# Kernel optimization log

Measured on AMD Instinct MI355X. Metric: run time of the kernel, lower is better.

## Reference

```python
import jax, jax.numpy as jnp
import numpy as np

N, E, D_IN, H, OUT = 50000, 800000, 128, 256, 2
BN_EPS = 1e-5
LN_EPS = 1e-5


def _xavier(k, fi, fo):
    lim = float(np.sqrt(6.0 / (fi + fo)))
    return jax.random.uniform(k, (fi, fo), minval=-lim, maxval=lim, dtype=jnp.float32)


def setup_inputs() -> dict:
    key = jax.random.key(0)
    ks = jax.random.split(key, 8)
    return {
        "x": jax.random.normal(ks[0], (N, D_IN), dtype=jnp.float32),
        "edge_index": jax.random.randint(ks[1], (2, E), 0, N, dtype=jnp.int32),
        "feature_scale": jnp.ones((D_IN,), jnp.float32),
        "feature_bias": jnp.zeros((D_IN,), jnp.float32),
        "bn0_g": jnp.ones((D_IN,), jnp.float32),
        "bn0_b": jnp.zeros((D_IN,), jnp.float32),
        "W1": _xavier(ks[2], D_IN, H), "b1": jnp.zeros((H,), jnp.float32),
        "bn1_g": jnp.ones((H,), jnp.float32), "bn1_b": jnp.zeros((H,), jnp.float32),
        "ln1_g": jnp.ones((H,), jnp.float32), "ln1_b": jnp.zeros((H,), jnp.float32),
        "W2": _xavier(ks[3], H, H), "b2": jnp.zeros((H,), jnp.float32),
        "bn2_g": jnp.ones((H,), jnp.float32), "bn2_b": jnp.zeros((H,), jnp.float32),
        "ln2_g": jnp.ones((H,), jnp.float32), "ln2_b": jnp.zeros((H,), jnp.float32),
        "Wout": _xavier(ks[4], H, OUT), "bout": jnp.zeros((OUT,), jnp.float32),
    }


def _batchnorm(x, g, b):
    # training-mode BatchNorm1d: batch stats over node axis, biased variance
    mu = jnp.mean(x, axis=0)
    var = jnp.mean(jnp.square(x - mu), axis=0)
    return g * (x - mu) * jax.lax.rsqrt(var + BN_EPS) + b


def _layernorm(x, g, b):
    mu = jnp.mean(x, axis=-1, keepdims=True)
    var = jnp.mean(jnp.square(x - mu), axis=-1, keepdims=True)
    return g * (x - mu) * jax.lax.rsqrt(var + LN_EPS) + b


def _gcn(x, W, b, src, dst, dinv):
    # PyG GCNConv with self-loops: D^{-1/2}(A+I)D^{-1/2} X W + b
    h = x @ W                                   # [N, F]
    norm = (dinv[src] * dinv[dst])[:, None]     # [E, 1]
    msg = h[src] * norm                         # [E, F] (dominant traffic)
    agg = jax.ops.segment_sum(msg, dst, num_segments=N)
    return agg + (dinv * dinv)[:, None] * h + b


def _forward(x, feature_scale, feature_bias, bn0_g, bn0_b,
             W1, b1, bn1_g, bn1_b, ln1_g, ln1_b,
             W2, b2, bn2_g, bn2_b, ln2_g, ln2_b,
             Wout, bout, edge_index):
    src, dst = edge_index[0], edge_index[1]
    deg = jax.ops.segment_sum(jnp.ones((E,), x.dtype), dst, num_segments=N) + 1.0
    dinv = jax.lax.rsqrt(deg)

    h = x * feature_scale + feature_bias
    h = _batchnorm(h, bn0_g, bn0_b)            # input_bn; dropout = identity (eval)

    # layer 0 (no residual: i == 0)
    h1 = _gcn(h, W1, b1, src, dst, dinv)
    h1 = jax.nn.relu(h1)
    h1 = _batchnorm(h1, bn1_g, bn1_b)
    h1 = _layernorm(h1, ln1_g, ln1_b)

    # layer 1 (residual add, shapes match)
    h2 = _gcn(h1, W2, b2, src, dst, dinv)
    h2 = jax.nn.relu(h2)
    h2 = _batchnorm(h2, bn2_g, bn2_b)
    h2 = _layernorm(h2, ln2_g, ln2_b)
    h2 = h2 + h1

    return h2 @ Wout + bout


def reference(x, edge_index, feature_scale, feature_bias, bn0_g, bn0_b,
              W1, b1, bn1_g, bn1_b, ln1_g, ln1_b,
              W2, b2, bn2_g, bn2_b, ln2_g, ln2_b,
              Wout, bout):
    return _forward(x, feature_scale, feature_bias, bn0_g, bn0_b,
                    W1, b1, bn1_g, bn1_b, ln1_g, ln1_b,
                    W2, b2, bn2_g, bn2_b, ln2_g, ln2_b,
                    Wout, bout, edge_index)
```

## Files before the change

### kernel.cpp

```cpp
#include <hip/hip_runtime.h>
#include <hip/hip_bf16.h>
#include <stdint.h>

#define N_NODES 50000
#define N_EDGES 800000
#define D_IN    128
#define H_DIM   256
#define BN_EPS  1e-5f
#define LN_EPS  1e-5f
#define NBLK2 782
#define SLICE_ELEMS ((size_t)N_NODES * 32)
#define EDGE_CHUNK 4096
#define BN0_BLOCKS 1024
#define TR_BLOCKS 256
#define NBKT 196
#define CHUNK 2048
#define RCHUNKS 391

typedef float v4f __attribute__((ext_vector_type(4)));
typedef float v2f __attribute__((ext_vector_type(2)));
typedef short v8s __attribute__((ext_vector_type(8)));
typedef unsigned v4u __attribute__((ext_vector_type(4)));

__device__ __forceinline__ float bflo(unsigned u){ return __uint_as_float(u << 16); }
__device__ __forceinline__ float bfhi(unsigned u){ return __uint_as_float(u & 0xffff0000u); }
__device__ __forceinline__ unsigned short f2bf(float f){
  unsigned u = __float_as_uint(f);
  u += 0x7fffu + ((u >> 16) & 1u);
  return (unsigned short)(u >> 16);
}
__device__ __forceinline__ unsigned pack2(float a, float b){
  return (unsigned)f2bf(a) | ((unsigned)f2bf(b) << 16);
}

__device__ __forceinline__ int block_excl_scan(int v){
  int t = threadIdx.x;
  int lane = t & 63, w = t >> 6;
  int inc = v;
  #pragma unroll
  for (int m = 1; m < 64; m <<= 1){
    int o = __shfl_up(inc, m, 64);
    if (lane >= m) inc += o;
  }
  __shared__ int wsum[4];
  if (lane == 63) wsum[w] = inc;
  __syncthreads();
  int base = 0;
  #pragma unroll
  for (int j = 0; j < 4; ++j) if (j < w) base += wsum[j];
  return base + inc - v;
}

__global__ __launch_bounds__(256) void bn0r1_k(const int* ei, const float* x,
                                               const float* fs, const float* fb,
                                               float* S, float* Q, int* ghist){
  int b = blockIdx.x, t = threadIdx.x;
  if (b >= BN0_BLOCKS){
    __shared__ int lh[NBKT];
    int b2 = b - BN0_BLOCKS;
    for (int i = t; i < NBKT; i += 256) lh[i] = 0;
    __syncthreads();
    int e0 = b2 * CHUNK;
    int n = min(CHUNK, N_EDGES - e0);
    for (int i = t; i < n; i += 256)
      atomicAdd(&lh[ei[N_EDGES + e0 + i] >> 8], 1);
    __syncthreads();
    if (t < NBKT && lh[t] > 0) atomicAdd(&ghist[t], lh[t]);
    return;
  }
  int cl = t & 31, rg = t >> 5;
  int c = cl * 4;
  float4 fs4 = *(const float4*)(fs + c);
  float4 fb4 = *(const float4*)(fb + c);
  float s0=0,s1=0,s2=0,s3=0,q0=0,q1=0,q2=0,q3=0;
  for (int row = b * 8 + rg; row < N_NODES; row += BN0_BLOCKS * 8){
    float4 xv = *(const float4*)(x + (size_t)row * D_IN + c);
    float v0 = xv.x * fs4.x + fb4.x;
    float v1 = xv.y * fs4.y + fb4.y;
    float v2 = xv.z * fs4.z + fb4.z;
    float v3 = xv.w * fs4.w + fb4.w;
    s0 += v0; s1 += v1; s2 += v2; s3 += v3;
    q0 += v0*v0; q1 += v1*v1; q2 += v2*v2; q3 += v3*v3;
  }
  __shared__ float red[256][8];
  red[t][0]=s0; red[t][1]=s1; red[t][2]=s2; red[t][3]=s3;
  red[t][4]=q0; red[t][5]=q1; red[t][6]=q2; red[t][7]=q3;
  __syncthreads();
  float* Sr = S + (b & 7) * D_IN;
  float* Qr = Q + (b & 7) * D_IN;
  if (t < 32){
    float a[8];
    #pragma unroll
    for (int i = 0; i < 8; ++i) a[i] = red[t][i];
    for (int j = 1; j < 8; ++j)
      #pragma unroll
      for (int i = 0; i < 8; ++i) a[i] += red[t + 32*j][i];
    #pragma unroll
    for (int i = 0; i < 4; ++i){ atomicAdd(&Sr[t*4+i], a[i]); atomicAdd(&Qr[t*4+i], a[4+i]); }
  }
}

__global__ __launch_bounds__(256) void r3_k(const int* ei, const int* ghist, int* gcursor, unsigned* ebuf){
  __shared__ unsigned short dstS[CHUNK];
  __shared__ int lh[NBKT], cb[NBKT], sbb[NBKT];
  int t = threadIdx.x;
  int v = (t < NBKT) ? ghist[t] : 0;
  int epre = block_excl_scan(v);
  if (t < NBKT){ sbb[t] = epre; lh[t] = 0; }
  __syncthreads();
  int e0 = blockIdx.x * CHUNK;
  int n = min(CHUNK, N_EDGES - e0);
  for (int i = t; i < n; i += 256){
    int d = ei[N_EDGES + e0 + i];
    dstS[i] = (unsigned short)d;
    atomicAdd(&lh[d >> 8], 1);
  }
  __syncthreads();
  if (t < NBKT && lh[t] > 0) cb[t] = sbb[t] + atomicAdd(&gcursor[t], lh[t]);
  __syncthreads();
  if (t < NBKT) lh[t] = 0;
  __syncthreads();
  for (int i = t; i < n; i += 256){
    int d = dstS[i];
    int bkt = d >> 8;
    int r = atomicAdd(&lh[bkt], 1);
    unsigned src = (unsigned)ei[e0 + i];
    ebuf[cb[bkt] + r] = ((unsigned)(d & 255) << 16) | src;
  }
}

__global__ __launch_bounds__(256) void sortprep_k(const unsigned* ebuf, const int* ghist,
                                                  int* perm, int* offs, float* dinv,
                                                  unsigned short* edges,
                                                  const float* W1, const float* W2,
                                                  unsigned short* W1t, unsigned short* W2t){
  int b = blockIdx.x, t = threadIdx.x;
  if (b < NBKT){
    __shared__ int h[256], dh[128], ep_s[128], W_s[128], lc[128], curs[256], sbb[NBKT + 1];
    int gv = (t < NBKT) ? ghist[t] : 0;
    int gpre = block_excl_scan(gv);
    if (t < NBKT) sbb[t] = gpre;
    if (t == NBKT - 1) sbb[NBKT] = gpre + gv;
    h[t] = 0;
    if (t < 128){ dh[t] = 0; lc[t] = 0; }
    __syncthreads();
    int lo = sbb[b], hi = sbb[b + 1];
    for (int i = lo + t; i < hi; i += 256)
      atomicAdd(&h[(ebuf[i] >> 16) & 255], 1);
    __syncthreads();
    int node = b * 256 + t;
    bool valid = node < N_NODES;
    int deg = valid ? h[t] : 0;
    if (valid) atomicAdd(&dh[min(deg, 127)], 1);
    __syncthreads();
    int cv = (t < 128) ? dh[t] : 0;
    int e1 = block_excl_scan(cv);
    __syncthreads();
    int e2 = block_excl_scan((t < 128) ? cv * t : 0);
    __syncthreads();
    if (t < 128){ ep_s[t] = e1; W_s[t] = e2; }
    __syncthreads();
    if (valid){
      int bin = min(deg, 127);
      int r = atomicAdd(&lc[bin], 1);
      int pl = ep_s[bin] + r;
      int pos = b * 256 + pl;
      int off = lo + W_s[bin] + (pl - ep_s[bin]) * deg;
      perm[pos] = node;
      offs[pos] = off;
      dinv[node] = rsqrtf((float)deg + 1.0f);
      curs[t] = off;
    }
    __syncthreads();
    for (int i = lo + t; i < hi; i += 256){
      unsigned u = ebuf[i];
      int l8 = (u >> 16) & 255;
      int pos = atomicAdd(&curs[l8], 1);
      edges[pos] = (unsigned short)(u & 0xffffu);
    }
    if (b == 0 && t == 0) offs[N_NODES] = N_EDGES;
    return;
  }
  int i = (b - NBKT) * 256 + t;
  if (i < D_IN * H_DIM){
    int r = i / H_DIM, c = i % H_DIM;
    W1t[c * D_IN + r] = f2bf(W1[i]);
  }
  if (i < H_DIM * H_DIM){
    int r = i / H_DIM, c = i % H_DIM;
    W2t[c * H_DIM + r] = f2bf(W2[i]);
  }
}

__global__ __launch_bounds__(256) void gemm1_k(const float* x, const float* S, const float* Q,
                                               const float* fs, const float* fb,
                                               const float* gg, const float* bb,
                                               const unsigned short* Bt, const float* dinv,
                                               unsigned short* C, int M){
  __shared__ __align__(16) short smem[18944];
  __shared__ float ac[128], cc[128], dvs[64];
  short* As = smem;
  short* Bs = smem + 64 * 136;
  int t = threadIdx.x;
  int m0 = blockIdx.x * 64;
  int lane = t & 63, w = t >> 6;
  int fr = lane & 15, quad = lane >> 4;
  if (t < 64) dvs[t] = (m0 + t < M) ? dinv[m0 + t] : 0.0f;
  if (t < 128){
    float s8 = 0.f, q8 = 0.f;
    #pragma unroll
    for (int rep = 0; rep < 8; ++rep){ s8 += S[rep * D_IN + t]; q8 += Q[rep * D_IN + t]; }
    const float invN = 1.0f / N_NODES;
    float mu = s8 * invN;
    float rs = rsqrtf(q8 * invN - mu * mu + BN_EPS);
    float a = gg[t] * rs * fs[t];
    ac[t] = a;
    cc[t] = gg[t] * rs * (fb[t] - mu) + bb[t];
  }
  __syncthreads();
  {
    int r = t >> 2, q = t & 3;
    int arow = m0 + r;
    #pragma unroll
    for (int j = 0; j < 4; ++j){
      int c = q * 32 + j * 8;
      float4 xv0 = {0,0,0,0}, xv1 = {0,0,0,0};
      if (arow < M){
        xv0 = *(const float4*)(x + (size_t)arow * D_IN + c);
        xv1 = *(const float4*)(x + (size_t)arow * D_IN + c + 4);
      }
      float4 a0 = *(const float4*)(&ac[c]);
      float4 a1 = *(const float4*)(&ac[c + 4]);
      float4 c0 = *(const float4*)(&cc[c]);
      float4 c1 = *(const float4*)(&cc[c + 4]);
      uint4 o;
      o.x = pack2(a0.x * xv0.x + c0.x, a0.y * xv0.y + c0.y);
      o.y = pack2(a0.z * xv0.z + c0.z, a0.w * xv0.w + c0.w);
      o.z = pack2(a1.x * xv1.x + c1.x, a1.y * xv1.y + c1.y);
      o.w = pack2(a1.z * xv1.z + c1.z, a1.w * xv1.w + c1.w);
      *(uint4*)(&As[r * 136 + c]) = o;
    }
  }
  v4f acc[4][4] = {};
  int sr = t >> 2;
  int sk = (t & 3) << 3;
  for (int k0 = 0; k0 < D_IN; k0 += 32){
    __syncthreads();
    #pragma unroll
    for (int j = 0; j < 4; ++j){
      int brow = sr + 64 * j;
      uint4 bv = *(const uint4*)(Bt + (size_t)brow * D_IN + k0 + sk);
      *(uint4*)(&Bs[brow * 40 + sk]) = bv;
    }
    __syncthreads();
    v8s af[4], bf[4];
    #pragma unroll
    for (int mi = 0; mi < 4; ++mi)
      af[mi] = *(const v8s*)(&As[(mi * 16 + fr) * 136 + k0 + quad * 8]);
    #pragma unroll
    for (int ni = 0; ni < 4; ++ni)
      bf[ni] = *(const v8s*)(&Bs[(w * 64 + ni * 16 + fr) * 40 + quad * 8]);
    #pragma unroll
    for (int mi = 0; mi < 4; ++mi)
      #pragma unroll
      for (int ni = 0; ni < 4; ++ni)
        acc[mi][ni] = __builtin_amdgcn_mfma_f32_16x16x32_bf16(af[mi], bf[ni], acc[mi][ni], 0, 0, 0);
  }
  __syncthreads();
  short* Cs = smem;
  #pragma unroll
  for (int mi = 0; mi < 4; ++mi)
    #pragma unroll
    for (int ni = 0; ni < 4; ++ni)
      #pragma unroll
      for (int r = 0; r < 4; ++r){
        int row = mi * 16 + quad * 4 + r;
        int col = w * 64 + ni * 16 + fr;
        Cs[row * 264 + col] = (short)f2bf(acc[mi][ni][r] * dvs[row]);
      }
  __syncthreads();
  int orow = t >> 2;
  int grow = m0 + orow;
  if (grow < M){
    #pragma unroll
    for (int j = 0; j < 4; ++j){
      int oc = (t & 3) * 16 + 64 * j;
      v8s v0 = *(const v8s*)(&Cs[orow * 264 + oc]);
      v8s v1 = *(const v8s*)(&Cs[orow * 264 + oc + 8]);
      *(v8s*)(&C[(size_t)(oc >> 5) * SLICE_ELEMS + (size_t)grow * 32 + (oc & 31)]) = v0;
      int oc1 = oc + 8;
      *(v8s*)(&C[(size_t)(oc1 >> 5) * SLICE_ELEMS + (size_t)grow * 32 + (oc1 & 31)]) = v1;
    }
  }
}

__global__ __launch_bounds__(256) void gemm2_k(const unsigned short* gB,
                                               const float* Sg, const float* Qg,
                                               const float* bng, const float* bnb,
                                               const float* lng, const float* lnb,
                                               const unsigned short* Bt, const float* dinv,
                                               unsigned short* C, unsigned short* h1, int M){
  __shared__ __align__(16) short smem[27136];
  __shared__ float scs[256], shs[256], dvs[64];
  short* As = smem;
  short* Bs = smem + 64 * 264;
  int t = threadIdx.x;
  int m0 = blockIdx.x * 64;
  int lane = t & 63, w = t >> 6;
  int fr = lane & 15, quad = lane >> 4;
  if (t < 64) dvs[t] = (m0 + t < M) ? dinv[m0 + t] : 0.0f;
  {
    const float invN = 1.0f / N_NODES;
    float mu = Sg[t] * invN;
    float rs = rsqrtf(Qg[t] * invN - mu * mu + BN_EPS);
    float s = bng[t] * rs;
    scs[t] = s; shs[t] = bnb[t] - s * mu;
  }
  __syncthreads();
  {
    int r = t >> 2, q = t & 3;
    int grow = m0 + r;
    int c0 = q * 64;
    float v[64];
    #pragma unroll
    for (int j = 0; j < 8; ++j){
      uint4 u = {0,0,0,0};
      int c = c0 + j * 8;
      if (grow < M) u = *(const uint4*)(gB + (size_t)grow * H_DIM + c);
      float4 s0 = *(const float4*)(&scs[c]);
      float4 s1 = *(const float4*)(&scs[c + 4]);
      float4 h0 = *(const float4*)(&shs[c]);
      float4 h4 = *(const float4*)(&shs[c + 4]);
      v[j*8+0] = s0.x * bflo(u.x) + h0.x;
      v[j*8+1] = s0.y * bfhi(u.x) + h0.y;
      v[j*8+2] = s0.z * bflo(u.y) + h0.z;
      v[j*8+3] = s0.w * bfhi(u.y) + h0.w;
      v[j*8+4] = s1.x * bflo(u.z) + h4.x;
      v[j*8+5] = s1.y * bfhi(u.z) + h4.y;
      v[j*8+6] = s1.z * bflo(u.w) + h4.z;
      v[j*8+7] = s1.w * bfhi(u.w) + h4.w;
    }
    float sum = 0.f, sq = 0.f;
    #pragma unroll
    for (int i = 0; i < 64; ++i){ sum += v[i]; sq += v[i] * v[i]; }
    sum += __shfl_xor(sum, 1, 64); sum += __shfl_xor(sum, 2, 64);
    sq  += __shfl_xor(sq, 1, 64);  sq  += __shfl_xor(sq, 2, 64);
    float mu = sum * (1.0f / H_DIM);
    float var = sq * (1.0f / H_DIM) - mu * mu;
    float rs = rsqrtf(var + LN_EPS);
    #pragma unroll
    for (int j = 0; j < 8; ++j){
      int c = c0 + j * 8;
      float4 g0 = *(const float4*)(lng + c);
      float4 g1 = *(const float4*)(lng + c + 4);
      float4 b0 = *(const float4*)(lnb + c);
      float4 b1 = *(const float4*)(lnb + c + 4);
      uint4 o;
      o.x = pack2(g0.x * (v[j*8+0] - mu) * rs + b0.x, g0.y * (v[j*8+1] - mu) * rs + b0.y);
      o.y = pack2(g0.z * (v[j*8+2] - mu) * rs + b0.z, g0.w * (v[j*8+3] - mu) * rs + b0.w);
      o.z = pack2(g1.x * (v[j*8+4] - mu) * rs + b1.x, g1.y * (v[j*8+5] - mu) * rs + b1.y);
      o.w = pack2(g1.z * (v[j*8+6] - mu) * rs + b1.z, g1.w * (v[j*8+7] - mu) * rs + b1.w);
      *(uint4*)(&As[r * 264 + c]) = o;
      if (grow < M) *(uint4*)(h1 + (size_t)grow * H_DIM + c) = o;
    }
  }
  v4f acc[4][4] = {};
  int sr = t >> 2;
  int sk = (t & 3) << 3;
  for (int k0 = 0; k0 < H_DIM; k0 += 32){
    __syncthreads();
    #pragma unroll
    for (int j = 0; j < 4; ++j){
      int brow = sr + 64 * j;
      uint4 bv = *(const uint4*)(Bt + (size_t)brow * H_DIM + k0 + sk);
      *(uint4*)(&Bs[brow * 40 + sk]) = bv;
    }
    __syncthreads();
    v8s af[4], bf[4];
    #pragma unroll
    for (int mi = 0; mi < 4; ++mi)
      af[mi] = *(const v8s*)(&As[(mi * 16 + fr) * 264 + k0 + quad * 8]);
    #pragma unroll
    for (int ni = 0; ni < 4; ++ni)
      bf[ni] = *(const v8s*)(&Bs[(w * 64 + ni * 16 + fr) * 40 + quad * 8]);
    #pragma unroll
    for (int mi = 0; mi < 4; ++mi)
      #pragma unroll
      for (int ni = 0; ni < 4; ++ni)
        acc[mi][ni] = __builtin_amdgcn_mfma_f32_16x16x32_bf16(af[mi], bf[ni], acc[mi][ni], 0, 0, 0);
  }
  __syncthreads();
  short* Cs = smem;
  #pragma unroll
  for (int mi = 0; mi < 4; ++mi)
    #pragma unroll
    for (int ni = 0; ni < 4; ++ni)
      #pragma unroll
      for (int r = 0; r < 4; ++r){
        int row = mi * 16 + quad * 4 + r;
        int col = w * 64 + ni * 16 + fr;
        Cs[row * 264 + col] = (short)f2bf(acc[mi][ni][r] * dvs[row]);
      }
  __syncthreads();
  int orow = t >> 2;
  int grow = m0 + orow;
  if (grow < M){
    #pragma unroll
    for (int j = 0; j < 4; ++j){
      int oc = (t & 3) * 16 + 64 * j;
      v8s v0 = *(const v8s*)(&Cs[orow * 264 + oc]);
      v8s v1 = *(const v8s*)(&Cs[orow * 264 + oc + 8]);
      *(v8s*)(&C[(size_t)(oc >> 5) * SLICE_ELEMS + (size_t)grow * 32 + (oc & 31)]) = v0;
      int oc1 = oc + 8;
      *(v8s*)(&C[(size_t)(oc1 >> 5) * SLICE_ELEMS + (size_t)grow * 32 + (oc1 & 31)]) = v1;
    }
  }
}

#define ACCP(u, A) { v2f d_ = {bflo(u), bfhi(u)}; A += d_; }
#define ACC8(vv) ACCP(vv.x, A0) ACCP(vv.y, A1) ACCP(vv.z, A2) ACCP(vv.w, A3)

__global__ __launch_bounds__(256, 4) void agg_k(const unsigned short* hs, const int* offsets,
                                                const unsigned short* edges, const int* perm,
                                                const float* dinv, const float* bias,
                                                unsigned short* g, float* pS, float* pQ){
  __shared__ unsigned eds32[EDGE_CHUNK / 2];
  __shared__ float wps[4][4][16];
  int t = threadIdx.x;
  int lane = t & 63;
  int wv = t >> 6;
  int slice = blockIdx.x & 7;
  int l4 = lane & 3;
  int grp = blockIdx.x >> 3;
  int nb = grp * 64;
  int idx = nb + (t >> 2);
  int lastn = min(nb + 64, N_NODES);
  int blk0 = offsets[nb];
  int base = blk0 & ~1;
  int blkN = offsets[lastn];
  const unsigned* gsrc = (const unsigned*)(edges + base);
  int nu = min((blkN - base + 1) >> 1, EDGE_CHUNK / 2);
  for (int i = t; i < nu; i += 256)
    eds32[i] = gsrc[i];
  __syncthreads();
  bool act = idx < N_NODES;
  int node = act ? perm[idx] : 0;
  float dvv = act ? dinv[node] : 0.f;
  const uint4* hb4 = (const uint4*)(hs + (size_t)slice * SLICE_ELEMS);
  float4 bb0 = *(const float4*)(bias + slice * 32 + l4 * 8);
  float4 bb1 = *(const float4*)(bias + slice * 32 + l4 * 8 + 4);
  uint4 sv = hb4[(size_t)node * 4 + l4];
  v2f A0 = {bflo(sv.x), bfhi(sv.x)};
  v2f A1 = {bflo(sv.y), bfhi(sv.y)};
  v2f A2 = {bflo(sv.z), bfhi(sv.z)};
  v2f A3 = {bflo(sv.w), bfhi(sv.w)};
  int e  = act ? offsets[idx] : 0;
  int e1 = act ? offsets[idx + 1] : 0;
  if ((e & 1) && e < e1){
    int ru = (e - base) >> 1;
    unsigned d = (ru < EDGE_CHUNK / 2) ? eds32[ru] : gsrc[ru];
    uint4 vv = hb4[(size_t)(d >> 16) * 4 + l4];
    ACC8(vv);
    ++e;
  }
  for (; e + 16 <= e1; e += 16){
    int ru = (e - base) >> 1;
    unsigned dd[8];
    if (ru + 8 <= EDGE_CHUNK / 2){
      #pragma unroll
      for (int j = 0; j < 8; ++j) dd[j] = eds32[ru + j];
    } else {
      #pragma unroll
      for (int j = 0; j < 8; ++j) dd[j] = gsrc[ru + j];
    }
    uint4 v[16];
    #pragma unroll
    for (int j = 0; j < 8; ++j){
      v[2*j]   = hb4[(size_t)(dd[j] & 0xffffu) * 4 + l4];
      v[2*j+1] = hb4[(size_t)(dd[j] >> 16)     * 4 + l4];
    }
    #pragma unroll
    for (int j = 0; j < 16; ++j){ ACC8(v[j]); }
  }
  if (e + 8 <= e1){
    int ru = (e - base) >> 1;
    unsigned dd[4];
    if (ru + 4 <= EDGE_CHUNK / 2){
      #pragma unroll
      for (int j = 0; j < 4; ++j) dd[j] = eds32[ru + j];
    } else {
      #pragma unroll
      for (int j = 0; j < 4; ++j) dd[j] = gsrc[ru + j];
    }
    uint4 v[8];
    #pragma unroll
    for (int j = 0; j < 4; ++j){
      v[2*j]   = hb4[(size_t)(dd[j] & 0xffffu) * 4 + l4];
      v[2*j+1] = hb4[(size_t)(dd[j] >> 16)     * 4 + l4];
    }
    #pragma unroll
    for (int j = 0; j < 8; ++j){ ACC8(v[j]); }
    e += 8;
  }
  if (e + 4 <= e1){
    int ru = (e - base) >> 1;
    unsigned dd0, dd1;
    if (ru + 2 <= EDGE_CHUNK / 2){
      dd0 = eds32[ru]; dd1 = eds32[ru + 1];
    } else {
      dd0 = gsrc[ru]; dd1 = gsrc[ru + 1];
    }
    uint4 v[4];
    v[0] = hb4[(size_t)(dd0 & 0xffffu) * 4 + l4];
    v[1] = hb4[(size_t)(dd0 >> 16)     * 4 + l4];
    v[2] = hb4[(size_t)(dd1 & 0xffffu) * 4 + l4];
    v[3] = hb4[(size_t)(dd1 >> 16)     * 4 + l4];
    #pragma unroll
    for (int j = 0; j < 4; ++j){ ACC8(v[j]); }
    e += 4;
  }
  for (; e < e1; ++e){
    int r = e - base;
    unsigned d = ((r >> 1) < EDGE_CHUNK / 2) ? eds32[r >> 1] : gsrc[r >> 1];
    unsigned s = (r & 1) ? (d >> 16) : (d & 0xffffu);
    uint4 vv = hb4[(size_t)s * 4 + l4];
    ACC8(vv);
  }
  float y0 = act ? fmaxf(dvv * A0.x + bb0.x, 0.f) : 0.f;
  float y1 = act ? fmaxf(dvv * A0.y + bb0.y, 0.f) : 0.f;
  float y2 = act ? fmaxf(dvv * A1.x + bb0.z, 0.f) : 0.f;
  float y3 = act ? fmaxf(dvv * A1.y + bb0.w, 0.f) : 0.f;
  float y4 = act ? fmaxf(dvv * A2.x + bb1.x, 0.f) : 0.f;
  float y5 = act ? fmaxf(dvv * A2.y + bb1.y, 0.f) : 0.f;
  float y6 = act ? fmaxf(dvv * A3.x + bb1.z, 0.f) : 0.f;
  float y7 = act ? fmaxf(dvv * A3.y + bb1.w, 0.f) : 0.f;
  if (act){
    v4u o;
    o.x = pack2(y0, y1); o.y = pack2(y2, y3);
    o.z = pack2(y4, y5); o.w = pack2(y6, y7);
    __builtin_nontemporal_store(o, (v4u*)(g + (size_t)node * H_DIM + slice * 32 + l4 * 8));
  }
  float q0 = y0*y0, q1 = y1*y1, q2 = y2*y2, q3 = y3*y3;
  float q4 = y4*y4, q5 = y5*y5, q6 = y6*y6, q7 = y7*y7;
  #pragma unroll
  for (int m = 4; m < 64; m <<= 1){
    y0 += __shfl_xor(y0, m, 64); y1 += __shfl_xor(y1, m, 64);
    y2 += __shfl_xor(y2, m, 64); y3 += __shfl_xor(y3, m, 64);
    y4 += __shfl_xor(y4, m, 64); y5 += __shfl_xor(y5, m, 64);
    y6 += __shfl_xor(y6, m, 64); y7 += __shfl_xor(y7, m, 64);
    q0 += __shfl_xor(q0, m, 64); q1 += __shfl_xor(q1, m, 64);
    q2 += __shfl_xor(q2, m, 64); q3 += __shfl_xor(q3, m, 64);
    q4 += __shfl_xor(q4, m, 64); q5 += __shfl_xor(q5, m, 64);
    q6 += __shfl_xor(q6, m, 64); q7 += __shfl_xor(q7, m, 64);
  }
  if (lane < 4){
    wps[wv][lane][0] = y0; wps[wv][lane][1] = y1; wps[wv][lane][2] = y2; wps[wv][lane][3] = y3;
    wps[wv][lane][4] = y4; wps[wv][lane][5] = y5; wps[wv][lane][6] = y6; wps[wv][lane][7] = y7;
    wps[wv][lane][8] = q0; wps[wv][lane][9] = q1; wps[wv][lane][10] = q2; wps[wv][lane][11] = q3;
    wps[wv][lane][12] = q4; wps[wv][lane][13] = q5; wps[wv][lane][14] = q6; wps[wv][lane][15] = q7;
  }
  __syncthreads();
  if (t < 64){
    int tl = t >> 4, ti = t & 15;
    float v = wps[0][tl][ti] + wps[1][tl][ti] + wps[2][tl][ti] + wps[3][tl][ti];
    int col32 = tl * 8 + (ti & 7);
    if (ti < 8) pS[(size_t)blockIdx.x * 32 + col32] = v;
    else        pQ[(size_t)blockIdx.x * 32 + col32] = v;
  }
}

__global__ __launch_bounds__(1024) void redu_k(const float* pS, const float* pQ,
                                               float* Sg, float* Qg){
  __shared__ float ls[32][32], lq[32][32];
  int t = threadIdx.x;
  int slice = blockIdx.x & 7;
  int part = blockIdx.x >> 3;
  int grp = t >> 5, c32 = t & 31;
  float as = 0.f, aq = 0.f;
  for (int b2 = part + grp * 8; b2 < NBLK2; b2 += 256){
    size_t o = ((size_t)b2 * 8 + slice) * 32 + c32;
    as += pS[o]; aq += pQ[o];
  }
  ls[grp][c32] = as; lq[grp][c32] = aq;
  __syncthreads();
  if (t < 32){
    float S = 0.f, Q = 0.f;
    #pragma unroll
    for (int gI = 0; gI < 32; ++gI){ S += ls[gI][t]; Q += lq[gI][t]; }
    atomicAdd(&Sg[slice * 32 + t], S);
    atomicAdd(&Qg[slice * 32 + t], Q);
  }
}

__global__ __launch_bounds__(256) void apply2_k(const unsigned short* g,
                                                const float* Sg, const float* Qg,
                                                const float* bng, const float* bnb,
                                                const float* lng, const float* lnb,
                                                const unsigned short* h1, const float* Wout,
                                                const float* bout, float* out){
  int t = threadIdx.x;
  int lane32 = t & 31;
  int row = blockIdx.x * 8 + (t >> 5);
  if (row >= N_NODES) return;
  int c = lane32 * 8;
  const float invN = 1.0f / N_NODES;
  float4 S0 = *(const float4*)(Sg + c), S1 = *(const float4*)(Sg + c + 4);
  float4 Q0 = *(const float4*)(Qg + c), Q1 = *(const float4*)(Qg + c + 4);
  float4 G0 = *(const float4*)(bng + c), G1 = *(const float4*)(bng + c + 4);
  float4 B0 = *(const float4*)(bnb + c), B1 = *(const float4*)(bnb + c + 4);
  float Sa[8] = {S0.x,S0.y,S0.z,S0.w,S1.x,S1.y,S1.z,S1.w};
  float Qa[8] = {Q0.x,Q0.y,Q0.z,Q0.w,Q1.x,Q1.y,Q1.z,Q1.w};
  float Ga[8] = {G0.x,G0.y,G0.z,G0.w,G1.x,G1.y,G1.z,G1.w};
  float Ba[8] = {B0.x,B0.y,B0.z,B0.w,B1.x,B1.y,B1.z,B1.w};
  float scv[8], shv[8];
  #pragma unroll
  for (int j = 0; j < 8; ++j){
    float mu = Sa[j] * invN;
    float rs = rsqrtf(Qa[j] * invN - mu * mu + BN_EPS);
    float s = Ga[j] * rs;
    scv[j] = s; shv[j] = Ba[j] - s * mu;
  }
  uint4 u = *(const uint4*)(g + (size_t)row * H_DIM + c);
  float v0 = scv[0] * bflo(u.x) + shv[0];
  float v1 = scv[1] * bfhi(u.x) + shv[1];
  float v2 = scv[2] * bflo(u.y) + shv[2];
  float v3 = scv[3] * bfhi(u.y) + shv[3];
  float v4 = scv[4] * bflo(u.z) + shv[4];
  float v5 = scv[5] * bfhi(u.z) + shv[5];
  float v6 = scv[6] * bflo(u.w) + shv[6];
  float v7 = scv[7] * bfhi(u.w) + shv[7];
  float sum = v0+v1+v2+v3+v4+v5+v6+v7;
  float sq  = v0*v0+v1*v1+v2*v2+v3*v3+v4*v4+v5*v5+v6*v6+v7*v7;
  #pragma unroll
  for (int m = 1; m < 32; m <<= 1){ sum += __shfl_xor(sum, m, 64); sq += __shfl_xor(sq, m, 64); }
  float mu = sum * (1.0f / H_DIM);
  float var = sq * (1.0f / H_DIM) - mu * mu;
  float rs = rsqrtf(var + LN_EPS);
  float4 g40 = *(const float4*)(lng + c);
  float4 g41 = *(const float4*)(lng + c + 4);
  float4 b40 = *(const float4*)(lnb + c);
  float4 b41 = *(const float4*)(lnb + c + 4);
  uint4 hr = *(const uint4*)(h1 + (size_t)row * H_DIM + c);
  float y0 = g40.x * (v0 - mu) * rs + b40.x + bflo(hr.x);
  float y1 = g40.y * (v1 - mu) * rs + b40.y + bfhi(hr.x);
  float y2 = g40.z * (v2 - mu) * rs + b40.z + bflo(hr.y);
  float y3 = g40.w * (v3 - mu) * rs + b40.w + bfhi(hr.y);
  float y4 = g41.x * (v4 - mu) * rs + b41.x + bflo(hr.z);
  float y5 = g41.y * (v5 - mu) * rs + b41.y + bfhi(hr.z);
  float y6 = g41.z * (v6 - mu) * rs + b41.z + bflo(hr.w);
  float y7 = g41.w * (v7 - mu) * rs + b41.w + bfhi(hr.w);
  float4 w0 = *(const float4*)(Wout + c * 2);
  float4 w1 = *(const float4*)(Wout + c * 2 + 4);
  float4 w2 = *(const float4*)(Wout + c * 2 + 8);
  float4 w3 = *(const float4*)(Wout + c * 2 + 12);
  float o0 = y0*w0.x + y1*w0.z + y2*w1.x + y3*w1.z + y4*w2.x + y5*w2.z + y6*w3.x + y7*w3.z;
  float o1 = y0*w0.y + y1*w0.w + y2*w1.y + y3*w1.w + y4*w2.y + y5*w2.w + y6*w3.y + y7*w3.w;
  #pragma unroll
  for (int m = 1; m < 32; m <<= 1){ o0 += __shfl_xor(o0, m, 64); o1 += __shfl_xor(o1, m, 64); }
  if (lane32 == 0){
    out[(size_t)row * 2 + 0] = o0 + bout[0];
    out[(size_t)row * 2 + 1] = o1 + bout[1];
  }
}

extern "C" void kernel_launch(void* const* d_in, const int* in_sizes, int n_in,
                              void* d_out, int out_size, void* d_ws, size_t ws_size,
                              hipStream_t stream) {
  const float* x    = (const float*)d_in[0];
  const int*   ei   = (const int*)d_in[1];
  const float* fs   = (const float*)d_in[2];
  const float* fb   = (const float*)d_in[3];
  const float* bn0g = (const float*)d_in[4];
  const float* bn0b = (const float*)d_in[5];
  const float* W1   = (const float*)d_in[6];
  const float* b1   = (const float*)d_in[7];
  const float* bn1g = (const float*)d_in[8];
  const float* bn1b = (const float*)d_in[9];
  const float* ln1g = (const float*)d_in[10];
  const float* ln1b = (const float*)d_in[11];
  const float* W2   = (const float*)d_in[12];
  const float* b2   = (const float*)d_in[13];
  const float* bn2g = (const float*)d_in[14];
  const float* bn2b = (const float*)d_in[15];
  const float* ln2g = (const float*)d_in[16];
  const float* ln2b = (const float*)d_in[17];
  const float* Wout = (const float*)d_in[18];
  const float* bout = (const float*)d_in[19];
  float* out = (float*)d_out;

  char* w = (char*)d_ws;
  float* bn0S  = (float*)(w + 0);
  float* bn0Q  = (float*)(w + 4096);
  int*   ghist  = (int*)(w + 8192);
  int*   gcursor= (int*)(w + 8976);
  float* Sg1   = (float*)(w + 9760);
  float* Qg1   = (float*)(w + 10784);
  float* Sg2   = (float*)(w + 11808);
  float* Qg2   = (float*)(w + 12832);
  const size_t ZERO_BYTES = 13856;
  float* dinv  = (float*)(w + 211584);
  int*   offs  = (int*)(w + 411584);
  int*   perm  = (int*)(w + 611712);
  unsigned short* edges = (unsigned short*)(w + 1011712);
  unsigned short* W1t  = (unsigned short*)(w + 15411712);
  unsigned short* W2t  = (unsigned short*)(w + 15477248);
  unsigned short* hlin = (unsigned short*)(w + 15608320);
  unsigned*       ebuf = (unsigned*)(w + 15608320);
  unsigned short* gbuf = (unsigned short*)(w + 41208320);
  unsigned short* h1   = (unsigned short*)(w + 66808320);
  float* pS    = (float*)(w + 92408320);
  float* pQ    = (float*)(w + 94008832);

  (void)in_sizes; (void)n_in; (void)out_size; (void)ws_size;

  hipMemsetAsync(d_ws, 0, ZERO_BYTES, stream);

  bn0r1_k<<<BN0_BLOCKS + RCHUNKS, 256, 0, stream>>>(ei, x, fs, fb, bn0S, bn0Q, ghist);
  r3_k<<<RCHUNKS, 256, 0, stream>>>(ei, ghist, gcursor, ebuf);
  sortprep_k<<<NBKT + TR_BLOCKS, 256, 0, stream>>>(
      ebuf, ghist, perm, offs, dinv, edges, W1, W2, W1t, W2t);

  int ggrid = (N_NODES + 63) / 64;
  int agg_blocks = NBLK2 * 8;

  gemm1_k<<<ggrid, 256, 0, stream>>>(x, bn0S, bn0Q, fs, fb, bn0g, bn0b, W1t, dinv, hlin, N_NODES);
  agg_k<<<agg_blocks, 256, 0, stream>>>(hlin, offs, edges, perm, dinv, b1, gbuf, pS, pQ);
  redu_k<<<64, 1024, 0, stream>>>(pS, pQ, Sg1, Qg1);

  gemm2_k<<<ggrid, 256, 0, stream>>>(gbuf, Sg1, Qg1, bn1g, bn1b, ln1g, ln1b, W2t, dinv, hlin, h1, N_NODES);
  agg_k<<<agg_blocks, 256, 0, stream>>>(hlin, offs, edges, perm, dinv, b2, gbuf, pS, pQ);
  redu_k<<<64, 1024, 0, stream>>>(pS, pQ, Sg2, Qg2);
  apply2_k<<<(N_NODES + 7) / 8, 256, 0, stream>>>(gbuf, Sg2, Qg2, bn2g, bn2b, ln2g, ln2b, h1, Wout, bout, out);
}
```

Before: 360.3 us.

## Split BN1/LN1 prologue out of gemm2 into separate apply kernel

Removes the fused batchnorm+layernorm prologue from the second GEMM and moves it into a standalone elementwise kernel that writes h1. The GEMM becomes a generic templated kernel that streams A tiles from global memory with a smaller shared-memory footprint, which may allow higher occupancy. The trade-off is an extra launch plus a full write and re-read of h1 (N×256 bf16) through global memory.

```diff
diff --git a/kernel.cpp b/kernel.cpp
--- a/kernel.cpp
+++ b/kernel.cpp
@@ -294,92 +294,39 @@
   }
 }
 
-__global__ __launch_bounds__(256) void gemm2_k(const unsigned short* gB,
-                                               const float* Sg, const float* Qg,
-                                               const float* bng, const float* bnb,
-                                               const float* lng, const float* lnb,
-                                               const unsigned short* Bt, const float* dinv,
-                                               unsigned short* C, unsigned short* h1, int M){
-  __shared__ __align__(16) short smem[27136];
-  __shared__ float scs[256], shs[256], dvs[64];
+template<int K>
+__global__ __launch_bounds__(256) void gemm_k(const unsigned short* A, const unsigned short* Bt,
+                                              const float* dinv, unsigned short* C, int M){
+  __shared__ __align__(16) short smem[16896];
+  __shared__ float dvs[64];
   short* As = smem;
-  short* Bs = smem + 64 * 264;
+  short* Bs = smem + 64 * 40;
   int t = threadIdx.x;
   int m0 = blockIdx.x * 64;
-  int lane = t & 63, w = t >> 6;
+  int lane = t & 63;
+  int w = t >> 6;
   int fr = lane & 15, quad = lane >> 4;
   if (t < 64) dvs[t] = (m0 + t < M) ? dinv[m0 + t] : 0.0f;
-  {
-    const float invN = 1.0f / N_NODES;
-    float mu = Sg[t] * invN;
-    float rs = rsqrtf(Qg[t] * invN - mu * mu + BN_EPS);
-    float s = bng[t] * rs;
-    scs[t] = s; shs[t] = bnb[t] - s * mu;
-  }
-  __syncthreads();
-  {
-    int r = t >> 2, q = t & 3;
-    int grow = m0 + r;
-    int c0 = q * 64;
-    float v[64];
-    #pragma unroll
-    for (int j = 0; j < 8; ++j){
-      uint4 u = {0,0,0,0};
-      int c = c0 + j * 8;
-      if (grow < M) u = *(const uint4*)(gB + (size_t)grow * H_DIM + c);
-      float4 s0 = *(const float4*)(&scs[c]);
-      float4 s1 = *(const float4*)(&scs[c + 4]);
-      float4 h0 = *(const float4*)(&shs[c]);
-      float4 h4 = *(const float4*)(&shs[c + 4]);
-      v[j*8+0] = s0.x * bflo(u.x) + h0.x;
-      v[j*8+1] = s0.y * bfhi(u.x) + h0.y;
-      v[j*8+2] = s0.z * bflo(u.y) + h0.z;
-      v[j*8+3] = s0.w * bfhi(u.y) + h0.w;
-      v[j*8+4] = s1.x * bflo(u.z) + h4.x;
-      v[j*8+5] = s1.y * bfhi(u.z) + h4.y;
-      v[j*8+6] = s1.z * bflo(u.w) + h4.z;
-      v[j*8+7] = s1.w * bfhi(u.w) + h4.w;
-    }
-    float sum = 0.f, sq = 0.f;
-    #pragma unroll
-    for (int i = 0; i < 64; ++i){ sum += v[i]; sq += v[i] * v[i]; }
-    sum += __shfl_xor(sum, 1, 64); sum += __shfl_xor(sum, 2, 64);
-    sq  += __shfl_xor(sq, 1, 64);  sq  += __shfl_xor(sq, 2, 64);
-    float mu = sum * (1.0f / H_DIM);
-    float var = sq * (1.0f / H_DIM) - mu * mu;
-    float rs = rsqrtf(var + LN_EPS);
-    #pragma unroll
-    for (int j = 0; j < 8; ++j){
-      int c = c0 + j * 8;
-      float4 g0 = *(const float4*)(lng + c);
-      float4 g1 = *(const float4*)(lng + c + 4);
-      float4 b0 = *(const float4*)(lnb + c);
-      float4 b1 = *(const float4*)(lnb + c + 4);
-      uint4 o;
-      o.x = pack2(g0.x * (v[j*8+0] - mu) * rs + b0.x, g0.y * (v[j*8+1] - mu) * rs + b0.y);
-      o.y = pack2(g0.z * (v[j*8+2] - mu) * rs + b0.z, g0.w * (v[j*8+3] - mu) * rs + b0.w);
-      o.z = pack2(g1.x * (v[j*8+4] - mu) * rs + b1.x, g1.y * (v[j*8+5] - mu) * rs + b1.y);
-      o.w = pack2(g1.z * (v[j*8+6] - mu) * rs + b1.z, g1.w * (v[j*8+7] - mu) * rs + b1.w);
-      *(uint4*)(&As[r * 264 + c]) = o;
-      if (grow < M) *(uint4*)(h1 + (size_t)grow * H_DIM + c) = o;
-    }
-  }
   v4f acc[4][4] = {};
   int sr = t >> 2;
   int sk = (t & 3) << 3;
-  for (int k0 = 0; k0 < H_DIM; k0 += 32){
-    __syncthreads();
+  for (int k0 = 0; k0 < K; k0 += 32){
+    __syncthreads();
+    uint4 av = {0,0,0,0};
+    int arow = m0 + sr;
+    if (arow < M) av = *(const uint4*)(A + (size_t)arow * K + k0 + sk);
+    *(uint4*)(&As[sr * 40 + sk]) = av;
     #pragma unroll
     for (int j = 0; j < 4; ++j){
       int brow = sr + 64 * j;
-      uint4 bv = *(const uint4*)(Bt + (size_t)brow * H_DIM + k0 + sk);
+      uint4 bv = *(const uint4*)(Bt + (size_t)brow * K + k0 + sk);
       *(uint4*)(&Bs[brow * 40 + sk]) = bv;
     }
     __syncthreads();
     v8s af[4], bf[4];
     #pragma unroll
     for (int mi = 0; mi < 4; ++mi)
-      af[mi] = *(const v8s*)(&As[(mi * 16 + fr) * 264 + k0 + quad * 8]);
+      af[mi] = *(const v8s*)(&As[(mi * 16 + fr) * 40 + quad * 8]);
     #pragma unroll
     for (int ni = 0; ni < 4; ++ni)
       bf[ni] = *(const v8s*)(&Bs[(w * 64 + ni * 16 + fr) * 40 + quad * 8]);
@@ -590,6 +537,60 @@
     atomicAdd(&Sg[slice * 32 + t], S);
     atomicAdd(&Qg[slice * 32 + t], Q);
   }
+}
+
+__global__ __launch_bounds__(256) void apply1_k(const unsigned short* g,
+                                                const float* Sg, const float* Qg,
+                                                const float* bng, const float* bnb,
+                                                const float* lng, const float* lnb, unsigned short* h1){
+  int t = threadIdx.x;
+  int lane32 = t & 31;
+  int row = blockIdx.x * 8 + (t >> 5);
+  if (row >= N_NODES) return;
+  int c = lane32 * 8;
+  const float invN = 1.0f / N_NODES;
+  float4 S0 = *(const float4*)(Sg + c), S1 = *(const float4*)(Sg + c + 4);
+  float4 Q0 = *(const float4*)(Qg + c), Q1 = *(const float4*)(Qg + c + 4);
+  float4 G0 = *(const float4*)(bng + c), G1 = *(const float4*)(bng + c + 4);
+  float4 B0 = *(const float4*)(bnb + c), B1 = *(const float4*)(bnb + c + 4);
+  float Sa[8] = {S0.x,S0.y,S0.z,S0.w,S1.x,S1.y,S1.z,S1.w};
+  float Qa[8] = {Q0.x,Q0.y,Q0.z,Q0.w,Q1.x,Q1.y,Q1.z,Q1.w};
+  float Ga[8] = {G0.x,G0.y,G0.z,G0.w,G1.x,G1.y,G1.z,G1.w};
+  float Ba[8] = {B0.x,B0.y,B0.z,B0.w,B1.x,B1.y,B1.z,B1.w};
+  float scv[8], shv[8];
+  #pragma unroll
+  for (int j = 0; j < 8; ++j){
+    float mu = Sa[j] * invN;
+    float rs = rsqrtf(Qa[j] * invN - mu * mu + BN_EPS);
+    float s = Ga[j] * rs;
+    scv[j] = s; shv[j] = Ba[j] - s * mu;
+  }
+  uint4 u = *(const uint4*)(g + (size_t)row * H_DIM + c);
+  float v0 = scv[0] * bflo(u.x) + shv[0];
+  float v1 = scv[1] * bfhi(u.x) + shv[1];
+  float v2 = scv[2] * bflo(u.y) + shv[2];
+  float v3 = scv[3] * bfhi(u.y) + shv[3];
+  float v4 = scv[4] * bflo(u.z) + shv[4];
+  float v5 = scv[5] * bfhi(u.z) + shv[5];
+  float v6 = scv[6] * bflo(u.w) + shv[6];
+  float v7 = scv[7] * bfhi(u.w) + shv[7];
+  float sum = v0+v1+v2+v3+v4+v5+v6+v7;
+  float sq  = v0*v0+v1*v1+v2*v2+v3*v3+v4*v4+v5*v5+v6*v6+v7*v7;
+  #pragma unroll
+  for (int m = 1; m < 32; m <<= 1){ sum += __shfl_xor(sum, m, 64); sq += __shfl_xor(sq, m, 64); }
+  float mu = sum * (1.0f / H_DIM);
+  float var = sq * (1.0f / H_DIM) - mu * mu;
+  float rs = rsqrtf(var + LN_EPS);
+  float4 g40 = *(const float4*)(lng + c);
+  float4 g41 = *(const float4*)(lng + c + 4);
+  float4 b40 = *(const float4*)(lnb + c);
+  float4 b41 = *(const float4*)(lnb + c + 4);
+  uint4 o;
+  o.x = pack2(g40.x * (v0 - mu) * rs + b40.x, g40.y * (v1 - mu) * rs + b40.y);
+  o.y = pack2(g40.z * (v2 - mu) * rs + b40.z, g40.w * (v3 - mu) * rs + b40.w);
+  o.z = pack2(g41.x * (v4 - mu) * rs + b41.x, g41.y * (v5 - mu) * rs + b41.y);
+  o.w = pack2(g41.z * (v6 - mu) * rs + b41.z, g41.w * (v7 - mu) * rs + b41.w);
+  *(uint4*)(h1 + (size_t)row * H_DIM + c) = o;
 }
 
 __global__ __launch_bounds__(256) void apply2_k(const unsigned short* g,
@@ -726,8 +727,9 @@
   gemm1_k<<<ggrid, 256, 0, stream>>>(x, bn0S, bn0Q, fs, fb, bn0g, bn0b, W1t, dinv, hlin, N_NODES);
   agg_k<<<agg_blocks, 256, 0, stream>>>(hlin, offs, edges, perm, dinv, b1, gbuf, pS, pQ);
   redu_k<<<64, 1024, 0, stream>>>(pS, pQ, Sg1, Qg1);
-
-  gemm2_k<<<ggrid, 256, 0, stream>>>(gbuf, Sg1, Qg1, bn1g, bn1b, ln1g, ln1b, W2t, dinv, hlin, h1, N_NODES);
+  apply1_k<<<(N_NODES + 7) / 8, 256, 0, stream>>>(gbuf, Sg1, Qg1, bn1g, bn1b, ln1g, ln1b, h1);
+
+  gemm_k<H_DIM><<<ggrid, 256, 0, stream>>>(h1, W2t, dinv, hlin, N_NODES);
   agg_k<<<agg_blocks, 256, 0, stream>>>(hlin, offs, edges, perm, dinv, b2, gbuf, pS, pQ);
   redu_k<<<64, 1024, 0, stream>>>(pS, pQ, Sg2, Qg2);
   apply2_k<<<(N_NODES + 7) / 8, 256, 0, stream>>>(gbuf, Sg2, Qg2, bn2g, bn2b, ln2g, ln2b, h1, Wout, bout, out);
```

After: 337.2 us. 6.4% less time.

## Stream normalized A tiles in gemm2 and fold stat reduction into agg atomics

Applied to the files above, without the earlier changes.

gemm2 no longer stages the full 64x256 normalized A block in LDS. It first computes the per-row LayerNorm statistics in one pass, then re-reads each 32-column slice of gB inside the k-loop and normalizes it on the fly into a small 64x40 tile. This shrinks LDS use and register pressure (the 64-float array is gone) to allow higher occupancy, at the cost of reading gB twice. Separately, the redu_k kernel and its partial-sum buffers are removed, and agg_k atomically adds its per-block BN sums directly into the global accumulators. This saves a launch and a round trip through memory, but adds atomic contention on 512 addresses from about 6000 blocks.

```diff
diff --git a/kernel.cpp b/kernel.cpp
--- a/kernel.cpp
+++ b/kernel.cpp
@@ -300,10 +300,10 @@
                                                const float* lng, const float* lnb,
                                                const unsigned short* Bt, const float* dinv,
                                                unsigned short* C, unsigned short* h1, int M){
-  __shared__ __align__(16) short smem[27136];
-  __shared__ float scs[256], shs[256], dvs[64];
+  __shared__ __align__(16) short smem[16896];
+  __shared__ float scs[256], shs[256], lgs[256], lbs[256], muS[64], rsS[64], dvs[64];
   short* As = smem;
-  short* Bs = smem + 64 * 264;
+  short* Bs = smem + 64 * 40;
   int t = threadIdx.x;
   int m0 = blockIdx.x * 64;
   int lane = t & 63, w = t >> 6;
@@ -315,53 +315,41 @@
     float rs = rsqrtf(Qg[t] * invN - mu * mu + BN_EPS);
     float s = bng[t] * rs;
     scs[t] = s; shs[t] = bnb[t] - s * mu;
+    lgs[t] = lng[t]; lbs[t] = lnb[t];
   }
   __syncthreads();
   {
     int r = t >> 2, q = t & 3;
     int grow = m0 + r;
-    int c0 = q * 64;
-    float v[64];
-    #pragma unroll
-    for (int j = 0; j < 8; ++j){
-      uint4 u = {0,0,0,0};
-      int c = c0 + j * 8;
-      if (grow < M) u = *(const uint4*)(gB + (size_t)grow * H_DIM + c);
-      float4 s0 = *(const float4*)(&scs[c]);
-      float4 s1 = *(const float4*)(&scs[c + 4]);
-      float4 h0 = *(const float4*)(&shs[c]);
-      float4 h4 = *(const float4*)(&shs[c + 4]);
-      v[j*8+0] = s0.x * bflo(u.x) + h0.x;
-      v[j*8+1] = s0.y * bfhi(u.x) + h0.y;
-      v[j*8+2] = s0.z * bflo(u.y) + h0.z;
-      v[j*8+3] = s0.w * bfhi(u.y) + h0.w;
-      v[j*8+4] = s1.x * bflo(u.z) + h4.x;
-      v[j*8+5] = s1.y * bfhi(u.z) + h4.y;
-      v[j*8+6] = s1.z * bflo(u.w) + h4.z;
-      v[j*8+7] = s1.w * bfhi(u.w) + h4.w;
-    }
     float sum = 0.f, sq = 0.f;
-    #pragma unroll
-    for (int i = 0; i < 64; ++i){ sum += v[i]; sq += v[i] * v[i]; }
+    if (grow < M){
+      #pragma unroll
+      for (int j = 0; j < 8; ++j){
+        int c = q * 64 + j * 8;
+        uint4 u = *(const uint4*)(gB + (size_t)grow * H_DIM + c);
+        float4 s0 = *(const float4*)(&scs[c]);
+        float4 s1 = *(const float4*)(&scs[c + 4]);
+        float4 h0 = *(const float4*)(&shs[c]);
+        float4 h4 = *(const float4*)(&shs[c + 4]);
+        float v0 = s0.x * bflo(u.x) + h0.x;
+        float v1 = s0.y * bfhi(u.x) + h0.y;
+        float v2 = s0.z * bflo(u.y) + h0.z;
+        float v3 = s0.w * bfhi(u.y) + h0.w;
+        float v4 = s1.x * bflo(u.z) + h4.x;
+        float v5 = s1.y * bfhi(u.z) + h4.y;
+        float v6 = s1.z * bflo(u.w) + h4.z;
+        float v7 = s1.w * bfhi(u.w) + h4.w;
+        sum += v0+v1+v2+v3+v4+v5+v6+v7;
+        sq  += v0*v0+v1*v1+v2*v2+v3*v3+v4*v4+v5*v5+v6*v6+v7*v7;
+      }
+    }
     sum += __shfl_xor(sum, 1, 64); sum += __shfl_xor(sum, 2, 64);
     sq  += __shfl_xor(sq, 1, 64);  sq  += __shfl_xor(sq, 2, 64);
-    float mu = sum * (1.0f / H_DIM);
-    float var = sq * (1.0f / H_DIM) - mu * mu;
-    float rs = rsqrtf(var + LN_EPS);
-    #pragma unroll
-    for (int j = 0; j < 8; ++j){
-      int c = c0 + j * 8;
-      float4 g0 = *(const float4*)(lng + c);
-      float4 g1 = *(const float4*)(lng + c + 4);
-      float4 b0 = *(const float4*)(lnb + c);
-      float4 b1 = *(const float4*)(lnb + c + 4);
-      uint4 o;
-      o.x = pack2(g0.x * (v[j*8+0] - mu) * rs + b0.x, g0.y * (v[j*8+1] - mu) * rs + b0.y);
-      o.y = pack2(g0.z * (v[j*8+2] - mu) * rs + b0.z, g0.w * (v[j*8+3] - mu) * rs + b0.w);
-      o.z = pack2(g1.x * (v[j*8+4] - mu) * rs + b1.x, g1.y * (v[j*8+5] - mu) * rs + b1.y);
-      o.w = pack2(g1.z * (v[j*8+6] - mu) * rs + b1.z, g1.w * (v[j*8+7] - mu) * rs + b1.w);
-      *(uint4*)(&As[r * 264 + c]) = o;
-      if (grow < M) *(uint4*)(h1 + (size_t)grow * H_DIM + c) = o;
+    if (q == 0){
+      float mu = sum * (1.0f / H_DIM);
+      float var = sq * (1.0f / H_DIM) - mu * mu;
+      muS[r] = mu;
+      rsS[r] = rsqrtf(var + LN_EPS);
     }
   }
   v4f acc[4][4] = {};
@@ -369,6 +357,35 @@
   int sk = (t & 3) << 3;
   for (int k0 = 0; k0 < H_DIM; k0 += 32){
     __syncthreads();
+    {
+      int arow = m0 + sr;
+      uint4 av = {0,0,0,0};
+      if (arow < M){
+        int c = k0 + sk;
+        uint4 u = *(const uint4*)(gB + (size_t)arow * H_DIM + c);
+        float mu = muS[sr], rs = rsS[sr];
+        float4 s0 = *(const float4*)(&scs[c]);
+        float4 s1 = *(const float4*)(&scs[c + 4]);
+        float4 h0 = *(const float4*)(&shs[c]);
+        float4 h4 = *(const float4*)(&shs[c + 4]);
+        float4 g0 = *(const float4*)(&lgs[c]);
+        float4 g1 = *(const float4*)(&lgs[c + 4]);
+        float4 b0 = *(const float4*)(&lbs[c]);
+        float4 b1 = *(const float4*)(&lbs[c + 4]);
+        float y0 = g0.x * ((s0.x * bflo(u.x) + h0.x) - mu) * rs + b0.x;
+        float y1 = g0.y * ((s0.y * bfhi(u.x) + h0.y) - mu) * rs + b0.y;
+        float y2 = g0.z * ((s0.z * bflo(u.y) + h0.z) - mu) * rs + b0.z;
+        float y3 = g0.w * ((s0.w * bfhi(u.y) + h0.w) - mu) * rs + b0.w;
+        float y4 = g1.x * ((s1.x * bflo(u.z) + h4.x) - mu) * rs + b1.x;
+        float y5 = g1.y * ((s1.y * bfhi(u.z) + h4.y) - mu) * rs + b1.y;
+        float y6 = g1.z * ((s1.z * bflo(u.w) + h4.z) - mu) * rs + b1.z;
+        float y7 = g1.w * ((s1.w * bfhi(u.w) + h4.w) - mu) * rs + b1.w;
+        av.x = pack2(y0, y1); av.y = pack2(y2, y3);
+        av.z = pack2(y4, y5); av.w = pack2(y6, y7);
+        *(uint4*)(h1 + (size_t)arow * H_DIM + c) = av;
+      }
+      *(uint4*)(&As[sr * 40 + sk]) = av;
+    }
     #pragma unroll
     for (int j = 0; j < 4; ++j){
       int brow = sr + 64 * j;
@@ -379,7 +396,7 @@
     v8s af[4], bf[4];
     #pragma unroll
     for (int mi = 0; mi < 4; ++mi)
-      af[mi] = *(const v8s*)(&As[(mi * 16 + fr) * 264 + k0 + quad * 8]);
+      af[mi] = *(const v8s*)(&As[(mi * 16 + fr) * 40 + quad * 8]);
     #pragma unroll
     for (int ni = 0; ni < 4; ++ni)
       bf[ni] = *(const v8s*)(&Bs[(w * 64 + ni * 16 + fr) * 40 + quad * 8]);
@@ -423,7 +440,7 @@
 __global__ __launch_bounds__(256, 4) void agg_k(const unsigned short* hs, const int* offsets,
                                                 const unsigned short* edges, const int* perm,
                                                 const float* dinv, const float* bias,
-                                                unsigned short* g, float* pS, float* pQ){
+                                                unsigned short* g, float* Sg, float* Qg){
   __shared__ unsigned eds32[EDGE_CHUNK / 2];
   __shared__ float wps[4][4][16];
   int t = threadIdx.x;
@@ -564,31 +581,8 @@
     int tl = t >> 4, ti = t & 15;
     float v = wps[0][tl][ti] + wps[1][tl][ti] + wps[2][tl][ti] + wps[3][tl][ti];
     int col32 = tl * 8 + (ti & 7);
-    if (ti < 8) pS[(size_t)blockIdx.x * 32 + col32] = v;
-    else        pQ[(size_t)blockIdx.x * 32 + col32] = v;
-  }
-}
-
-__global__ __launch_bounds__(1024) void redu_k(const float* pS, const float* pQ,
-                                               float* Sg, float* Qg){
-  __shared__ float ls[32][32], lq[32][32];
-  int t = threadIdx.x;
-  int slice = blockIdx.x & 7;
-  int part = blockIdx.x >> 3;
-  int grp = t >> 5, c32 = t & 31;
-  float as = 0.f, aq = 0.f;
-  for (int b2 = part + grp * 8; b2 < NBLK2; b2 += 256){
-    size_t o = ((size_t)b2 * 8 + slice) * 32 + c32;
-    as += pS[o]; aq += pQ[o];
-  }
-  ls[grp][c32] = as; lq[grp][c32] = aq;
-  __syncthreads();
-  if (t < 32){
-    float S = 0.f, Q = 0.f;
-    #pragma unroll
-    for (int gI = 0; gI < 32; ++gI){ S += ls[gI][t]; Q += lq[gI][t]; }
-    atomicAdd(&Sg[slice * 32 + t], S);
-    atomicAdd(&Qg[slice * 32 + t], Q);
+    if (ti < 8) atomicAdd(&Sg[slice * 32 + col32], v);
+    else        atomicAdd(&Qg[slice * 32 + col32], v);
   }
 }
 
@@ -708,8 +702,6 @@
   unsigned*       ebuf = (unsigned*)(w + 15608320);
   unsigned short* gbuf = (unsigned short*)(w + 41208320);
   unsigned short* h1   = (unsigned short*)(w + 66808320);
-  float* pS    = (float*)(w + 92408320);
-  float* pQ    = (float*)(w + 94008832);
 
   (void)in_sizes; (void)n_in; (void)out_size; (void)ws_size;
 
@@ -724,11 +716,9 @@
   int agg_blocks = NBLK2 * 8;
 
   gemm1_k<<<ggrid, 256, 0, stream>>>(x, bn0S, bn0Q, fs, fb, bn0g, bn0b, W1t, dinv, hlin, N_NODES);
-  agg_k<<<agg_blocks, 256, 0, stream>>>(hlin, offs, edges, perm, dinv, b1, gbuf, pS, pQ);
-  redu_k<<<64, 1024, 0, stream>>>(pS, pQ, Sg1, Qg1);
+  agg_k<<<agg_blocks, 256, 0, stream>>>(hlin, offs, edges, perm, dinv, b1, gbuf, Sg1, Qg1);
 
   gemm2_k<<<ggrid, 256, 0, stream>>>(gbuf, Sg1, Qg1, bn1g, bn1b, ln1g, ln1b, W2t, dinv, hlin, h1, N_NODES);
-  agg_k<<<agg_blocks, 256, 0, stream>>>(hlin, offs, edges, perm, dinv, b2, gbuf, pS, pQ);
-  redu_k<<<64, 1024, 0, stream>>>(pS, pQ, Sg2, Qg2);
+  agg_k<<<agg_blocks, 256, 0, stream>>>(hlin, offs, edges, perm, dinv, b2, gbuf, Sg2, Qg2);
   apply2_k<<<(N_NODES + 7) / 8, 256, 0, stream>>>(gbuf, Sg2, Qg2, bn2g, bn2b, ln2g, ln2b, h1, Wout, bout, out);
 }
```

Measured after the change: 334.6 us. 1.08x faster.
